# Optimization experiments

Hardware: AMD Instinct MI355X
Metric: run time of the kernel (lower is better)

The kernel has to match this reference:

```python
import jax, jax.numpy as jnp
import numpy as np


def setup_inputs() -> dict:
    key = jax.random.key(0)
    k1, k2 = jax.random.split(key)
    B, T, D = 16, 4096, 1024
    hidden_states = jax.random.normal(k1, (B, T, D), dtype=jnp.float32)
    mask = jnp.ones((B, T), dtype=jnp.int32)
    context_vector = jax.random.normal(k2, (D,), dtype=jnp.float32)
    return {"hidden_states": hidden_states, "mask": mask, "context_vector": context_vector}


def reference(hidden_states, mask, context_vector):
    # scores: (B, T) dot of each token with learned context vector
    scores = jnp.einsum("btd,d->bt", hidden_states, context_vector)
    scores = jnp.where(mask == 0, -jnp.inf, scores)
    attn_weights = jax.nn.softmax(scores, axis=-1)  # (B, T)
    pooled = jnp.einsum("bt,btd->bd", attn_weights, hidden_states)
    return pooled
```

## Files before the change

### kernel.cpp

```cpp
#include <hip/hip_runtime.h>
#include <math.h>


typedef float f32x4 __attribute__((ext_vector_type(4)));

__global__ __launch_bounds__(256) void ap_partial(
    const float* __restrict__ hs, const int* __restrict__ mask,
    const float* __restrict__ ctx,
    float* __restrict__ accs, float* __restrict__ ms, float* __restrict__ ls,
    int T, int blocksPerB, int tokensPerWave)
{
    const int D = 1024;
    int bi    = blockIdx.x;
    int b     = bi / blocksPerB;
    int chunk = bi - b * blocksPerB;
    int wave  = threadIdx.x >> 6;
    int lane  = threadIdx.x & 63;
    int tid   = threadIdx.x;

    int t0 = chunk * (tokensPerWave * 4) + wave * tokensPerWave;

    const f32x4* ctx4 = (const f32x4*)ctx;
    f32x4 c0 = ctx4[0 * 64 + lane];
    f32x4 c1 = ctx4[1 * 64 + lane];
    f32x4 c2 = ctx4[2 * 64 + lane];
    f32x4 c3 = ctx4[3 * 64 + lane];

    f32x4 a0 = {0.f,0.f,0.f,0.f}, a1 = {0.f,0.f,0.f,0.f};
    f32x4 a2 = {0.f,0.f,0.f,0.f}, a3 = {0.f,0.f,0.f,0.f};
    float m = -INFINITY, l = 0.0f;

    const f32x4* hp = (const f32x4*)hs + ((size_t)b * T + t0) * (D / 4);
    const int*   mp = mask + (size_t)b * T + t0;

    for (int g = 0; g < tokensPerWave; g += 4) {
        f32x4 h[4][4];
        #pragma unroll
        for (int t = 0; t < 4; ++t) {
            const f32x4* row = hp + (size_t)(g + t) * (D / 4);
            #pragma unroll
            for (int j = 0; j < 4; ++j) h[t][j] = row[j * 64 + lane];
        }
        int4 mk4 = *(const int4*)(mp + g);

        float s0, s1, s2, s3;
        {
            float p, q;
            p = 0.f; q = 0.f;
            #pragma unroll
            for (int e = 0; e < 4; ++e) {
                p = fmaf(h[0][0][e], c0[e], p); q = fmaf(h[0][1][e], c1[e], q);
                p = fmaf(h[0][2][e], c2[e], p); q = fmaf(h[0][3][e], c3[e], q);
            }
            s0 = p + q;
            p = 0.f; q = 0.f;
            #pragma unroll
            for (int e = 0; e < 4; ++e) {
                p = fmaf(h[1][0][e], c0[e], p); q = fmaf(h[1][1][e], c1[e], q);
                p = fmaf(h[1][2][e], c2[e], p); q = fmaf(h[1][3][e], c3[e], q);
            }
            s1 = p + q;
            p = 0.f; q = 0.f;
            #pragma unroll
            for (int e = 0; e < 4; ++e) {
                p = fmaf(h[2][0][e], c0[e], p); q = fmaf(h[2][1][e], c1[e], q);
                p = fmaf(h[2][2][e], c2[e], p); q = fmaf(h[2][3][e], c3[e], q);
            }
            s2 = p + q;
            p = 0.f; q = 0.f;
            #pragma unroll
            for (int e = 0; e < 4; ++e) {
                p = fmaf(h[3][0][e], c0[e], p); q = fmaf(h[3][1][e], c1[e], q);
                p = fmaf(h[3][2][e], c2[e], p); q = fmaf(h[3][3][e], c3[e], q);
            }
            s3 = p + q;
        }

        #pragma unroll
        for (int off = 32; off > 0; off >>= 1) {
            float u0 = __shfl_xor(s0, off);
            float u1 = __shfl_xor(s1, off);
            float u2 = __shfl_xor(s2, off);
            float u3 = __shfl_xor(s3, off);
            s0 += u0; s1 += u1; s2 += u2; s3 += u3;
        }

        if (mk4.x != 0) {
            if (s0 > m) { float cc = __expf(m - s0); l *= cc; a0 *= cc; a1 *= cc; a2 *= cc; a3 *= cc; m = s0; }
            float w = __expf(s0 - m); l += w;
            a0 += w * h[0][0]; a1 += w * h[0][1]; a2 += w * h[0][2]; a3 += w * h[0][3];
        }
        if (mk4.y != 0) {
            if (s1 > m) { float cc = __expf(m - s1); l *= cc; a0 *= cc; a1 *= cc; a2 *= cc; a3 *= cc; m = s1; }
            float w = __expf(s1 - m); l += w;
            a0 += w * h[1][0]; a1 += w * h[1][1]; a2 += w * h[1][2]; a3 += w * h[1][3];
        }
        if (mk4.z != 0) {
            if (s2 > m) { float cc = __expf(m - s2); l *= cc; a0 *= cc; a1 *= cc; a2 *= cc; a3 *= cc; m = s2; }
            float w = __expf(s2 - m); l += w;
            a0 += w * h[2][0]; a1 += w * h[2][1]; a2 += w * h[2][2]; a3 += w * h[2][3];
        }
        if (mk4.w != 0) {
            if (s3 > m) { float cc = __expf(m - s3); l *= cc; a0 *= cc; a1 *= cc; a2 *= cc; a3 *= cc; m = s3; }
            float w = __expf(s3 - m); l += w;
            a0 += w * h[3][0]; a1 += w * h[3][1]; a2 += w * h[3][2]; a3 += w * h[3][3];
        }
    }

    __shared__ float s_m[4];
    __shared__ float s_lf[4];
    __shared__ f32x4 s_acc[4][256];

    if (lane == 0) s_m[wave] = m;
    __syncthreads();
    float M = fmaxf(fmaxf(s_m[0], s_m[1]), fmaxf(s_m[2], s_m[3]));
    float f = (m == -INFINITY) ? 0.0f : __expf(m - M);
    if (lane == 0) s_lf[wave] = l * f;
    s_acc[wave][0 * 64 + lane] = a0 * f;
    s_acc[wave][1 * 64 + lane] = a1 * f;
    s_acc[wave][2 * 64 + lane] = a2 * f;
    s_acc[wave][3 * 64 + lane] = a3 * f;
    __syncthreads();

    f32x4 v0 = s_acc[0][tid], v1 = s_acc[1][tid], v2 = s_acc[2][tid], v3 = s_acc[3][tid];
    f32x4 r = (v0 + v1) + (v2 + v3);

    f32x4* accs4 = (f32x4*)(accs + (size_t)bi * D);
    accs4[tid] = r;
    if (tid == 0) {
        ms[bi] = M;
        ls[bi] = (s_lf[0] + s_lf[1]) + (s_lf[2] + s_lf[3]);
    }
}

__global__ __launch_bounds__(256) void ap_combine(
    const float* __restrict__ accs, const float* __restrict__ ms,
    const float* __restrict__ ls, float* __restrict__ out, int numChunks)
{
    int b   = blockIdx.x;
    int tid = threadIdx.x;
    const float* mB = ms + (size_t)b * numChunks;
    const float* lB = ls + (size_t)b * numChunks;

    float M = -INFINITY;
    for (int c = 0; c < numChunks; ++c) M = fmaxf(M, mB[c]);
    float L = 0.0f;
    for (int c = 0; c < numChunks; ++c) {
        float mc = mB[c];
        float fc = (mc == -INFINITY) ? 0.0f : __expf(mc - M);
        L += lB[c] * fc;
    }

    f32x4 racc = {0.f,0.f,0.f,0.f};
    const f32x4* accs4 = (const f32x4*)accs;
    for (int c = 0; c < numChunks; ++c) {
        float mc = mB[c];
        float fc = (mc == -INFINITY) ? 0.0f : __expf(mc - M);
        f32x4 v = accs4[((size_t)b * numChunks + c) * 256 + tid];
        racc.x = fmaf(v.x, fc, racc.x); racc.y = fmaf(v.y, fc, racc.y);
        racc.z = fmaf(v.z, fc, racc.z); racc.w = fmaf(v.w, fc, racc.w);
    }
    float inv = 1.0f / L;
    ((f32x4*)out)[(size_t)b * 256 + tid] = racc * inv;
}

extern "C" void kernel_launch(void* const* d_in, const int* in_sizes, int n_in,
                              void* d_out, int out_size, void* d_ws, size_t ws_size,
                              hipStream_t stream)
{
    const float* hs   = (const float*)d_in[0];
    const int*   mask = (const int*)d_in[1];
    const float* ctx  = (const float*)d_in[2];

    const int D = 1024;
    int B = out_size / D;
    int T = in_sizes[1] / B;

    int blocksPerB = 128;
    while (blocksPerB > 1 &&
           ((T % (16 * blocksPerB)) != 0 ||
            (size_t)B * blocksPerB * (size_t)(D + 2) * sizeof(float) > ws_size))
        blocksPerB >>= 1;
    int tokensPerWave = T / (4 * blocksPerB);
    int numP = B * blocksPerB;

    float* accs = (float*)d_ws;
    float* ms   = accs + (size_t)numP * D;
    float* ls   = ms + numP;

    ap_partial<<<numP, 256, 0, stream>>>(hs, mask, ctx, accs, ms, ls,
                                         T, blocksPerB, tokensPerWave);
    ap_combine<<<B, 256, 0, stream>>>(accs, ms, ls, (float*)d_out, blocksPerB);
}
```

Baseline: 401.8 us.

## Stream hidden rows through an LDS ring via async global-to-LDS loads

Each wave now prefetches token rows three steps ahead into a four-slot per-wave LDS ring using global_load_lds, with explicit vmcnt waits, and processes one token at a time from LDS. The mask is loaded once per wave and broadcast with shuffles. The block count per batch now prefers 32, which gives 32 tokens per wave. The aim is to keep more memory requests in flight and hide load latency. In exchange it uses 64KB of LDS per block, which limits occupancy, and adds an LDS round trip plus serialized per-token reductions.

```diff
diff --git a/kernel.cpp b/kernel.cpp
--- a/kernel.cpp
+++ b/kernel.cpp
@@ -3,6 +3,14 @@
 
 
 typedef float f32x4 __attribute__((ext_vector_type(4)));
+
+using as1_void = __attribute__((address_space(1))) void;
+using as3_void = __attribute__((address_space(3))) void;
+
+__device__ __forceinline__ void gload_lds16(const void* g, void* l) {
+    __builtin_amdgcn_global_load_lds((as1_void*)(void*)(const_cast<void*>(g)),
+                                     (as3_void*)(l), 16, 0, 0);
+}
 
 __global__ __launch_bounds__(256) void ap_partial(
     const float* __restrict__ hs, const int* __restrict__ mask,
@@ -17,8 +25,13 @@
     int wave  = threadIdx.x >> 6;
     int lane  = threadIdx.x & 63;
     int tid   = threadIdx.x;
+    int TW    = tokensPerWave;
 
-    int t0 = chunk * (tokensPerWave * 4) + wave * tokensPerWave;
+    int t0 = chunk * (TW * 4) + wave * TW;
+
+    __shared__ char  smem[65536];
+    __shared__ float s_m[4];
+    __shared__ float s_lf[4];
 
     const f32x4* ctx4 = (const f32x4*)ctx;
     f32x4 c0 = ctx4[0 * 64 + lane];
@@ -26,103 +39,83 @@
     f32x4 c2 = ctx4[2 * 64 + lane];
     f32x4 c3 = ctx4[3 * 64 + lane];
 
+    const float* hp = hs + ((size_t)b * T + t0) * D;
+    const int*   mp = mask + (size_t)b * T + t0;
+    int mymask = mp[lane < TW ? lane : 0];
+
     f32x4 a0 = {0.f,0.f,0.f,0.f}, a1 = {0.f,0.f,0.f,0.f};
     f32x4 a2 = {0.f,0.f,0.f,0.f}, a3 = {0.f,0.f,0.f,0.f};
     float m = -INFINITY, l = 0.0f;
 
-    const f32x4* hp = (const f32x4*)hs + ((size_t)b * T + t0) * (D / 4);
-    const int*   mp = mask + (size_t)b * T + t0;
+    char* ringbase = smem + wave * 16384;
 
-    for (int g = 0; g < tokensPerWave; g += 4) {
-        f32x4 h[4][4];
+    auto stage = [&](int t) {
+        const float* rp = hp + (size_t)t * D + lane * 4;
+        char* lb = ringbase + (t & 3) * 4096;
+        gload_lds16(rp,       lb);
+        gload_lds16(rp + 256, lb + 1024);
+        gload_lds16(rp + 512, lb + 2048);
+        gload_lds16(rp + 768, lb + 3072);
+    };
+
+    auto compute = [&](int t) {
+        const f32x4* sp = (const f32x4*)(ringbase + (t & 3) * 4096);
+        f32x4 h0 = sp[0 * 64 + lane];
+        f32x4 h1 = sp[1 * 64 + lane];
+        f32x4 h2 = sp[2 * 64 + lane];
+        f32x4 h3 = sp[3 * 64 + lane];
+        float p = 0.f, q = 0.f;
         #pragma unroll
-        for (int t = 0; t < 4; ++t) {
-            const f32x4* row = hp + (size_t)(g + t) * (D / 4);
-            #pragma unroll
-            for (int j = 0; j < 4; ++j) h[t][j] = row[j * 64 + lane];
+        for (int e = 0; e < 4; ++e) {
+            p = fmaf(h0[e], c0[e], p); q = fmaf(h1[e], c1[e], q);
+            p = fmaf(h2[e], c2[e], p); q = fmaf(h3[e], c3[e], q);
         }
-        int4 mk4 = *(const int4*)(mp + g);
+        float s = p + q;
+        #pragma unroll
+        for (int off = 32; off > 0; off >>= 1) s += __shfl_xor(s, off);
+        int mk = __shfl(mymask, t);
+        if (mk != 0) {
+            if (s > m) {
+                float cc = __expf(m - s);
+                l *= cc; a0 *= cc; a1 *= cc; a2 *= cc; a3 *= cc; m = s;
+            }
+            float w = __expf(s - m); l += w;
+            a0 += w * h0; a1 += w * h1; a2 += w * h2; a3 += w * h3;
+        }
+    };
 
-        float s0, s1, s2, s3;
-        {
-            float p, q;
-            p = 0.f; q = 0.f;
-            #pragma unroll
-            for (int e = 0; e < 4; ++e) {
-                p = fmaf(h[0][0][e], c0[e], p); q = fmaf(h[0][1][e], c1[e], q);
-                p = fmaf(h[0][2][e], c2[e], p); q = fmaf(h[0][3][e], c3[e], q);
-            }
-            s0 = p + q;
-            p = 0.f; q = 0.f;
-            #pragma unroll
-            for (int e = 0; e < 4; ++e) {
-                p = fmaf(h[1][0][e], c0[e], p); q = fmaf(h[1][1][e], c1[e], q);
-                p = fmaf(h[1][2][e], c2[e], p); q = fmaf(h[1][3][e], c3[e], q);
-            }
-            s1 = p + q;
-            p = 0.f; q = 0.f;
-            #pragma unroll
-            for (int e = 0; e < 4; ++e) {
-                p = fmaf(h[2][0][e], c0[e], p); q = fmaf(h[2][1][e], c1[e], q);
-                p = fmaf(h[2][2][e], c2[e], p); q = fmaf(h[2][3][e], c3[e], q);
-            }
-            s2 = p + q;
-            p = 0.f; q = 0.f;
-            #pragma unroll
-            for (int e = 0; e < 4; ++e) {
-                p = fmaf(h[3][0][e], c0[e], p); q = fmaf(h[3][1][e], c1[e], q);
-                p = fmaf(h[3][2][e], c2[e], p); q = fmaf(h[3][3][e], c3[e], q);
-            }
-            s3 = p + q;
-        }
+    asm volatile("s_waitcnt vmcnt(0)" ::: "memory");
 
-        #pragma unroll
-        for (int off = 32; off > 0; off >>= 1) {
-            float u0 = __shfl_xor(s0, off);
-            float u1 = __shfl_xor(s1, off);
-            float u2 = __shfl_xor(s2, off);
-            float u3 = __shfl_xor(s3, off);
-            s0 += u0; s1 += u1; s2 += u2; s3 += u3;
-        }
+    stage(0); stage(1); stage(2);
+    int t = 0;
+    for (; t < TW - 3; ++t) {
+        stage(t + 3);
+        asm volatile("s_waitcnt vmcnt(12)" ::: "memory");
+        compute(t);
+    }
+    asm volatile("s_waitcnt vmcnt(8)" ::: "memory");
+    compute(t); ++t;
+    asm volatile("s_waitcnt vmcnt(4)" ::: "memory");
+    compute(t); ++t;
+    asm volatile("s_waitcnt vmcnt(0)" ::: "memory");
+    compute(t);
 
-        if (mk4.x != 0) {
-            if (s0 > m) { float cc = __expf(m - s0); l *= cc; a0 *= cc; a1 *= cc; a2 *= cc; a3 *= cc; m = s0; }
-            float w = __expf(s0 - m); l += w;
-            a0 += w * h[0][0]; a1 += w * h[0][1]; a2 += w * h[0][2]; a3 += w * h[0][3];
-        }
-        if (mk4.y != 0) {
-            if (s1 > m) { float cc = __expf(m - s1); l *= cc; a0 *= cc; a1 *= cc; a2 *= cc; a3 *= cc; m = s1; }
-            float w = __expf(s1 - m); l += w;
-            a0 += w * h[1][0]; a1 += w * h[1][1]; a2 += w * h[1][2]; a3 += w * h[1][3];
-        }
-        if (mk4.z != 0) {
-            if (s2 > m) { float cc = __expf(m - s2); l *= cc; a0 *= cc; a1 *= cc; a2 *= cc; a3 *= cc; m = s2; }
-            float w = __expf(s2 - m); l += w;
-            a0 += w * h[2][0]; a1 += w * h[2][1]; a2 += w * h[2][2]; a3 += w * h[2][3];
-        }
-        if (mk4.w != 0) {
-            if (s3 > m) { float cc = __expf(m - s3); l *= cc; a0 *= cc; a1 *= cc; a2 *= cc; a3 *= cc; m = s3; }
-            float w = __expf(s3 - m); l += w;
-            a0 += w * h[3][0]; a1 += w * h[3][1]; a2 += w * h[3][2]; a3 += w * h[3][3];
-        }
-    }
-
-    __shared__ float s_m[4];
-    __shared__ float s_lf[4];
-    __shared__ f32x4 s_acc[4][256];
+    __syncthreads();
+    f32x4* s_acc = (f32x4*)smem;
 
     if (lane == 0) s_m[wave] = m;
     __syncthreads();
     float M = fmaxf(fmaxf(s_m[0], s_m[1]), fmaxf(s_m[2], s_m[3]));
     float f = (m == -INFINITY) ? 0.0f : __expf(m - M);
     if (lane == 0) s_lf[wave] = l * f;
-    s_acc[wave][0 * 64 + lane] = a0 * f;
-    s_acc[wave][1 * 64 + lane] = a1 * f;
-    s_acc[wave][2 * 64 + lane] = a2 * f;
-    s_acc[wave][3 * 64 + lane] = a3 * f;
+    s_acc[wave * 256 + 0 * 64 + lane] = a0 * f;
+    s_acc[wave * 256 + 1 * 64 + lane] = a1 * f;
+    s_acc[wave * 256 + 2 * 64 + lane] = a2 * f;
+    s_acc[wave * 256 + 3 * 64 + lane] = a3 * f;
     __syncthreads();
 
-    f32x4 v0 = s_acc[0][tid], v1 = s_acc[1][tid], v2 = s_acc[2][tid], v3 = s_acc[3][tid];
+    f32x4 v0 = s_acc[0 * 256 + tid], v1 = s_acc[1 * 256 + tid];
+    f32x4 v2 = s_acc[2 * 256 + tid], v3 = s_acc[3 * 256 + tid];
     f32x4 r = (v0 + v1) + (v2 + v3);
 
     f32x4* accs4 = (f32x4*)(accs + (size_t)bi * D);
@@ -176,11 +169,17 @@
     int B = out_size / D;
     int T = in_sizes[1] / B;
 
-    int blocksPerB = 128;
-    while (blocksPerB > 1 &&
-           ((T % (16 * blocksPerB)) != 0 ||
-            (size_t)B * blocksPerB * (size_t)(D + 2) * sizeof(float) > ws_size))
-        blocksPerB >>= 1;
+    const int cand[5] = {32, 64, 16, 128, 8};
+    int blocksPerB = 0;
+    for (int i = 0; i < 5; ++i) {
+        int p  = cand[i];
+        if (T % (4 * p) != 0) continue;
+        int tw = T / (4 * p);
+        if (tw < 4 || tw > 64) continue;
+        if ((size_t)B * p * (size_t)(D + 2) * sizeof(float) > ws_size) continue;
+        blocksPerB = p; break;
+    }
+    if (blocksPerB == 0) blocksPerB = T / 128;
     int tokensPerWave = T / (4 * blocksPerB);
     int numP = B * blocksPerB;
 
```

After: 376.2 us. -6.4%, faster.
